# Optimization experiments

Hardware: AMD Instinct MI355X
Metric: run time of the kernel (lower is better)

## Reference

```python
import jax, jax.numpy as jnp
import numpy as np

N_NODES = 50000
N_EDGES = 1_600_000
IN_DIM = 128
HID = 32
HEADS = 4
NEG_SLOPE = 0.2


def setup_inputs() -> dict:
    key = jax.random.key(0)
    ks = jax.random.split(key, 6)
    h = jax.random.normal(ks[0], (N_NODES, IN_DIM), dtype=jnp.float32)
    src = jax.random.randint(ks[1], (N_EDGES,), 0, N_NODES, dtype=jnp.int32)
    dst = jax.random.randint(ks[2], (N_EDGES,), 0, N_NODES, dtype=jnp.int32)
    s = 1.0 / np.sqrt(IN_DIM)  # ~ Linear default init scale
    Wq = (jax.random.normal(ks[3], (HEADS, IN_DIM, HID), dtype=jnp.float32) * s)
    Wk = (jax.random.normal(ks[4], (HEADS, IN_DIM, HID), dtype=jnp.float32) * s)
    Wv = (jax.random.normal(ks[5], (HEADS, IN_DIM, HID), dtype=jnp.float32) * s)
    return {"h": h, "src": src, "dst": dst, "Wq": Wq, "Wk": Wk, "Wv": Wv}


def _gat_forward(h, src, dst, Wq, Wk, Wv):
    n = h.shape[0]
    # per-head projections: [H, N, D]
    q = jnp.einsum('ni,hio->hno', h, Wq)
    k = jnp.einsum('ni,hio->hno', h, Wk)
    v = jnp.einsum('ni,hio->hno', h, Wv)
    # edge scores: e = leaky_relu(<q_src, k_dst>)  -> [H, E]
    e = jax.nn.leaky_relu(jnp.einsum('hed,hed->he', q[:, src], k[:, dst]),
                          negative_slope=NEG_SLOPE)
    # segment softmax over incoming edges of each dst node
    seg_max = jax.vmap(lambda x: jax.ops.segment_max(x, dst, num_segments=n))(e)
    seg_max = jax.lax.stop_gradient(jnp.where(jnp.isfinite(seg_max), seg_max, 0.0))
    ex = jnp.exp(e - seg_max[:, dst])                       # [H, E]
    denom = jax.vmap(lambda x: jax.ops.segment_sum(x, dst, num_segments=n))(ex)
    alpha = ex / jnp.maximum(denom, 1e-9)[:, dst]           # [H, E]
    # weighted scatter-sum of source values into dst nodes: [H, N, D]
    msg = alpha[..., None] * v[:, src]
    out = jax.vmap(lambda m: jax.ops.segment_sum(m, dst, num_segments=n))(msg)
    # concat heads along feature dim -> [N, H*D]
    return out.transpose(1, 0, 2).reshape(n, HEADS * HID)


def reference(h, src, dst, Wq, Wk, Wv):
    return _gat_forward(h, src, dst, Wq, Wk, Wv)
```

## Files before the change

### kernel.cpp

```cpp
#include <hip/hip_runtime.h>
#include <hip/hip_fp16.h>

#define IN_DIM 128
#define HID 32
#define HEADS 4
#define OUTC (HEADS*HID)
#define NEG_SLOPE 0.2f
#define BSHIFT 7
#define BNODES 128
#define BCAP 6144
#define MAXBUCK 512
#define NCOLS 384
#define SUBN 16
#define SCAP 1024

typedef _Float16 f16x8 __attribute__((ext_vector_type(8)));
typedef float    f32x4 __attribute__((ext_vector_type(4)));

__device__ __forceinline__ unsigned short f2h(float f) {
    return __half_as_ushort(__float2half_rn(f));
}
__device__ __forceinline__ float2 h2f2(unsigned u) {
    __half2 h = *reinterpret_cast<__half2*>(&u);
    return __half22float2(h);
}
__device__ __forceinline__ float qdot(const uint4& qv, const float4& kd) {
    float2 a = h2f2(qv.x);
    float2 b = h2f2(qv.y);
    return a.x * kd.x + a.y * kd.y + b.x * kd.z + b.y * kd.w;
}
__device__ __forceinline__ void vacc(const uint4& qv, float e, float4& acc) {
    float2 a = h2f2(qv.z);
    float2 b = h2f2(qv.w);
    acc.x = fmaf(e, a.x, acc.x);
    acc.y = fmaf(e, a.y, acc.y);
    acc.z = fmaf(e, b.x, acc.z);
    acc.w = fmaf(e, b.y, acc.w);
}

__global__ __launch_bounds__(256) void w_prep(
    const float* __restrict__ Wq, const float* __restrict__ Wk,
    const float* __restrict__ Wv, unsigned short* __restrict__ Wt,
    int* __restrict__ gcount)
{
    int idx = blockIdx.x * 256 + threadIdx.x;
    if (idx < MAXBUCK) gcount[idx] = 0;
    if (idx >= NCOLS * IN_DIM) return;
    int c = idx >> 7, k = idx & 127;
    int sel = c >> 7;
    int cc  = c & 127;
    int head = cc >> 5, dcol = cc & 31;
    const float* W = (sel == 0) ? Wk : (sel == 1) ? Wq : Wv;
    Wt[idx] = f2h(W[(size_t)head * IN_DIM * HID + (size_t)k * HID + dcol]);
}

__global__ __launch_bounds__(256) void gat_proj_mfma(
    const float* __restrict__ h, const unsigned short* __restrict__ Wt,
    float* __restrict__ Ko, unsigned short* __restrict__ QV, int n)
{
    __shared__ unsigned short hsm[32 * IN_DIM];
    const int tid  = threadIdx.x;
    const int row0 = blockIdx.x * 32;

    for (int idx = tid; idx < 32 * 64; idx += 256) {
        int r  = idx >> 6;
        int c2 = idx & 63;
        int gr = row0 + r;
        float2 hv = (gr < n) ? ((const float2*)h)[(size_t)gr * 64 + c2]
                             : make_float2(0.f, 0.f);
        int col = c2 * 2;
        int sc  = col ^ ((r & 7) << 3);
        __half2 packed = __floats2half2_rn(hv.x, hv.y);
        *(unsigned*)&hsm[r * IN_DIM + sc] = *(unsigned*)&packed;
    }
    __syncthreads();

    const int w = tid >> 6;
    const int l = tid & 63;
    const int l15 = l & 15;
    const int kg  = l >> 4;
    const _Float16* Wt16 = (const _Float16*)Wt;

    f32x4 acc[2][6];
#pragma unroll
    for (int rt = 0; rt < 2; ++rt)
#pragma unroll
        for (int ct = 0; ct < 6; ++ct) acc[rt][ct] = (f32x4){0.f, 0.f, 0.f, 0.f};

#pragma unroll
    for (int s = 0; s < 4; ++s) {
        int scol = (s * 32 + kg * 8) ^ ((l & 7) << 3);
        f16x8 a0 = *(const f16x8*)&hsm[l15 * IN_DIM + scol];
        f16x8 a1 = *(const f16x8*)&hsm[(l15 + 16) * IN_DIM + scol];
#pragma unroll
        for (int ct = 0; ct < 6; ++ct) {
            int c = w * 96 + ct * 16 + l15;
            f16x8 b = *(const f16x8*)&Wt16[(size_t)c * IN_DIM + s * 32 + kg * 8];
            acc[0][ct] = __builtin_amdgcn_mfma_f32_16x16x32_f16(a0, b, acc[0][ct], 0, 0, 0);
            acc[1][ct] = __builtin_amdgcn_mfma_f32_16x16x32_f16(a1, b, acc[1][ct], 0, 0, 0);
        }
    }

#pragma unroll
    for (int rt = 0; rt < 2; ++rt) {
#pragma unroll
        for (int ct = 0; ct < 6; ++ct) {
            int cD = w * 96 + ct * 16 + l15;
#pragma unroll
            for (int r = 0; r < 4; ++r) {
                int node = row0 + rt * 16 + kg * 4 + r;
                if (node >= n) continue;
                float v = acc[rt][ct][r];
                if (cD < 128) {
                    Ko[(size_t)node * OUTC + cD] = v;
                } else if (cD < 256) {
                    int cq = cD - 128;
                    QV[(size_t)node * 256 + (cq >> 2) * 8 + (cq & 3)] = f2h(v);
                } else {
                    int cv = cD - 256;
                    QV[(size_t)node * 256 + (cv >> 2) * 8 + (cv & 3) + 4] = f2h(v);
                }
            }
        }
    }
}

__global__ __launch_bounds__(256) void gat_bin(
    const int* __restrict__ src, const int* __restrict__ dst,
    int* __restrict__ gcount, unsigned* __restrict__ pairs,
    int ne, int nbuck)
{
    __shared__ int hist[MAXBUCK];
    __shared__ int base[MAXBUCK];
    const int tid = threadIdx.x;
    for (int i = tid; i < nbuck; i += 256) hist[i] = 0;
    __syncthreads();

    const int ne4 = ne >> 2;
    const int4* s4 = (const int4*)src;
    const int4* d4 = (const int4*)dst;

    int4 sv[4], dv[4];
    int loc[16], bk[16];
    bool val[4];
#pragma unroll
    for (int k = 0; k < 4; ++k) {
        int idx = blockIdx.x * 1024 + k * 256 + tid;
        val[k] = idx < ne4;
        if (val[k]) { sv[k] = s4[idx]; dv[k] = d4[idx]; }
        else { sv[k] = make_int4(0,0,0,0); dv[k] = make_int4(0,0,0,0); }
    }
#pragma unroll
    for (int k = 0; k < 4; ++k) {
        int dd[4] = { dv[k].x, dv[k].y, dv[k].z, dv[k].w };
#pragma unroll
        for (int j = 0; j < 4; ++j) {
            int b = dd[j] >> BSHIFT;
            bk[k*4+j]  = b;
            loc[k*4+j] = val[k] ? atomicAdd(&hist[b], 1) : 0;
        }
    }
    __syncthreads();
    for (int i = tid; i < nbuck; i += 256)
        base[i] = hist[i] ? atomicAdd(&gcount[i], hist[i]) : 0;
    __syncthreads();
#pragma unroll
    for (int k = 0; k < 4; ++k) {
        if (!val[k]) continue;
        int ss[4] = { sv[k].x, sv[k].y, sv[k].z, sv[k].w };
        int dd[4] = { dv[k].x, dv[k].y, dv[k].z, dv[k].w };
#pragma unroll
        for (int j = 0; j < 4; ++j) {
            int b = bk[k*4+j];
            int p = base[b] + loc[k*4+j];
            if (p < BCAP)
                pairs[(size_t)b * BCAP + p] =
                    ((unsigned)ss[j] << BSHIFT) | (unsigned)(dd[j] & (BNODES-1));
        }
    }
    if (blockIdx.x == 0 && tid == 0) {
        for (int e = ne4 * 4; e < ne; ++e) {
            int b = dst[e] >> BSHIFT;
            int p = atomicAdd(&gcount[b], 1);
            if (p < BCAP)
                pairs[(size_t)b * BCAP + p] =
                    ((unsigned)src[e] << BSHIFT) | (unsigned)(dst[e] & (BNODES-1));
        }
    }
}

__global__ __launch_bounds__(256) void gat_bucket(
    const unsigned* __restrict__ pairs, const int* __restrict__ gcount,
    const uint4* __restrict__ QV, const float4* __restrict__ K4,
    float* __restrict__ out, int n, int nbuck)
{
    __shared__ unsigned short sl[SCAP];
    __shared__ int cl[SUBN], cur[SUBN], off[SUBN + 1];

    const int blk = blockIdx.x;
    const int sub = (blk >> 3) & 7;
    const int b   = (blk >> 6) * 8 + (blk & 7);
    if (b >= nbuck) return;
    const int tid = threadIdx.x;

    if (tid < SUBN) cl[tid] = 0;
    __syncthreads();

    int m = gcount[b]; if (m > BCAP) m = BCAP;
    const unsigned* pb = pairs + (size_t)b * BCAP;

    for (int i = tid; i < m; i += 256) {
        int dl = pb[i] & (BNODES - 1);
        if ((dl >> 4) == sub) atomicAdd(&cl[dl & (SUBN - 1)], 1);
    }
    __syncthreads();
    if (tid == 0) {
        int acc = 0;
#pragma unroll
        for (int i = 0; i < SUBN; ++i) { off[i] = acc; cur[i] = acc; acc += cl[i]; }
        off[SUBN] = acc;
    }
    __syncthreads();
    for (int i = tid; i < m; i += 256) {
        unsigned p = pb[i];
        int dl = p & (BNODES - 1);
        if ((dl >> 4) == sub) {
            int pos = atomicAdd(&cur[dl & (SUBN - 1)], 1);
            if (pos < SCAP) sl[pos] = (unsigned short)(p >> BSHIFT);
        }
    }
    __syncthreads();

    const int w    = tid >> 6;
    const int lane = tid & 63;
    const int l32  = lane & 31;
    const int g    = lane >> 5;

#pragma unroll
    for (int q = 0; q < SUBN / 4; ++q) {
        int nl   = q * 4 + w;
        int node = b * BNODES + sub * SUBN + nl;
        if (node >= n) continue;

        const int e0  = off[nl];
        const int deg = off[nl + 1] - e0;
        const float4 kd = K4[(size_t)node * 32 + l32];

        float4 acc = make_float4(0.f, 0.f, 0.f, 0.f);
        float  dsum = 0.f;

        const int half0 = (deg + 1) >> 1;
        int j  = e0 + (g ? half0 : 0);
        const int je = e0 + (g ? deg : half0);

        for (; j + 3 < je; j += 4) {
            int s0 = sl[j], s1 = sl[j + 1], s2 = sl[j + 2], s3 = sl[j + 3];
            uint4 w0 = QV[(size_t)s0 * 32 + l32];
            uint4 w1 = QV[(size_t)s1 * 32 + l32];
            uint4 w2 = QV[(size_t)s2 * 32 + l32];
            uint4 w3 = QV[(size_t)s3 * 32 + l32];

            float p0 = qdot(w0, kd), p1 = qdot(w1, kd);
            float p2 = qdot(w2, kd), p3 = qdot(w3, kd);
#pragma unroll
            for (int off2 = 1; off2 < 8; off2 <<= 1) {
                p0 += __shfl_xor(p0, off2, 8);
                p1 += __shfl_xor(p1, off2, 8);
                p2 += __shfl_xor(p2, off2, 8);
                p3 += __shfl_xor(p3, off2, 8);
            }
            float e0f = __expf(p0 > 0.f ? p0 : NEG_SLOPE * p0);
            float e1f = __expf(p1 > 0.f ? p1 : NEG_SLOPE * p1);
            float e2f = __expf(p2 > 0.f ? p2 : NEG_SLOPE * p2);
            float e3f = __expf(p3 > 0.f ? p3 : NEG_SLOPE * p3);
            dsum += (e0f + e1f) + (e2f + e3f);
            vacc(w0, e0f, acc); vacc(w1, e1f, acc);
            vacc(w2, e2f, acc); vacc(w3, e3f, acc);
        }
        for (; j < je; ++j) {
            int s0 = sl[j];
            uint4 w0 = QV[(size_t)s0 * 32 + l32];
            float p0 = qdot(w0, kd);
#pragma unroll
            for (int off2 = 1; off2 < 8; off2 <<= 1) p0 += __shfl_xor(p0, off2, 8);
            float e0f = __expf(p0 > 0.f ? p0 : NEG_SLOPE * p0);
            dsum += e0f;
            vacc(w0, e0f, acc);
        }

        acc.x += __shfl_xor(acc.x, 32, 64);
        acc.y += __shfl_xor(acc.y, 32, 64);
        acc.z += __shfl_xor(acc.z, 32, 64);
        acc.w += __shfl_xor(acc.w, 32, 64);
        dsum  += __shfl_xor(dsum, 32, 64);

        if (g == 0) {
            float inv = 1.f / fmaxf(dsum, 1e-9f);
            float4 o; o.x = acc.x*inv; o.y = acc.y*inv; o.z = acc.z*inv; o.w = acc.w*inv;
            ((float4*)out)[(size_t)node * 32 + l32] = o;
        }
    }
}

extern "C" void kernel_launch(void* const* d_in, const int* in_sizes, int n_in,
                              void* d_out, int out_size, void* d_ws, size_t ws_size,
                              hipStream_t stream) {
    const float* h   = (const float*)d_in[0];
    const int*   src = (const int*)d_in[1];
    const int*   dst = (const int*)d_in[2];
    const float* Wq  = (const float*)d_in[3];
    const float* Wk  = (const float*)d_in[4];
    const float* Wv  = (const float*)d_in[5];
    float* out = (float*)d_out;

    const int n     = in_sizes[0] / IN_DIM;
    const int ne    = in_sizes[1];
    const int nbuck = (n + BNODES - 1) >> BSHIFT;

    float*          K      = (float*)d_ws;
    unsigned short* QV     = (unsigned short*)(K + (size_t)n * OUTC);
    int*            gcount = (int*)(QV + (size_t)n * 256);
    unsigned*       pairs  = (unsigned*)(gcount + MAXBUCK);
    unsigned short* Wt     = (unsigned short*)(pairs + (size_t)MAXBUCK * BCAP);

    w_prep<<<(NCOLS * IN_DIM + 255) / 256, 256, 0, stream>>>(Wq, Wk, Wv, Wt, gcount);
    gat_proj_mfma<<<(n + 31) / 32, 256, 0, stream>>>(h, Wt, K, QV, n);

    int ne4 = ne >> 2;
    int binblk = (ne4 + 1023) / 1024;
    gat_bin<<<binblk, 256, 0, stream>>>(src, dst, gcount, pairs, ne, nbuck);

    int nb8  = (nbuck + 7) / 8;
    gat_bucket<<<nb8 * 64, 256, 0, stream>>>(pairs, gcount, (const uint4*)QV,
                                             (const float4*)K, out, n, nbuck);
}
```

Measured before the change: 183.7 us.

## Bin edges into 16-node buckets and fuse weight prep with binning

Edges are now binned directly into 16-node buckets (3125 buckets), so each gat_bucket block handles exactly one bucket. Before, each block rescanned a 128-node bucket and filtered for its 16-node sub-range, which made every bucket's pairs be read eight times. The weight conversion and the edge binning are merged into one launch, and the count reset moves to a memset. The cost is a larger shared histogram (3200 entries of hist plus base) and more global atomics on gcount during binning, which may lower occupancy in the binning blocks. The per-bucket capacity of 768 for 16 nodes averaging 512 edges leaves less slack for overflow.

```diff
diff --git a/kernel.cpp b/kernel.cpp
--- a/kernel.cpp
+++ b/kernel.cpp
@@ -6,13 +6,12 @@
 #define HEADS 4
 #define OUTC (HEADS*HID)
 #define NEG_SLOPE 0.2f
-#define BSHIFT 7
-#define BNODES 128
-#define BCAP 6144
-#define MAXBUCK 512
+#define BSH 4
+#define BN 16
+#define BCAP 768
+#define NBMAX 3200
 #define NCOLS 384
-#define SUBN 16
-#define SCAP 1024
+#define WPB 192
 
 typedef _Float16 f16x8 __attribute__((ext_vector_type(8)));
 typedef float    f32x4 __attribute__((ext_vector_type(4)));
@@ -38,20 +37,86 @@
     acc.w = fmaf(e, b.y, acc.w);
 }
 
-__global__ __launch_bounds__(256) void w_prep(
+__global__ __launch_bounds__(256) void prep_bin(
     const float* __restrict__ Wq, const float* __restrict__ Wk,
     const float* __restrict__ Wv, unsigned short* __restrict__ Wt,
-    int* __restrict__ gcount)
+    const int* __restrict__ src, const int* __restrict__ dst,
+    int* __restrict__ gcount, unsigned* __restrict__ pairs,
+    int ne, int nbuck)
 {
-    int idx = blockIdx.x * 256 + threadIdx.x;
-    if (idx < MAXBUCK) gcount[idx] = 0;
-    if (idx >= NCOLS * IN_DIM) return;
-    int c = idx >> 7, k = idx & 127;
-    int sel = c >> 7;
-    int cc  = c & 127;
-    int head = cc >> 5, dcol = cc & 31;
-    const float* W = (sel == 0) ? Wk : (sel == 1) ? Wq : Wv;
-    Wt[idx] = f2h(W[(size_t)head * IN_DIM * HID + (size_t)k * HID + dcol]);
+    const int tid = threadIdx.x;
+
+    if (blockIdx.x < WPB) {
+        int idx = blockIdx.x * 256 + tid;
+        if (idx < NCOLS * IN_DIM) {
+            int c = idx >> 7, k = idx & 127;
+            int sel = c >> 7;
+            int cc  = c & 127;
+            int head = cc >> 5, dcol = cc & 31;
+            const float* W = (sel == 0) ? Wk : (sel == 1) ? Wq : Wv;
+            Wt[idx] = f2h(W[(size_t)head * IN_DIM * HID + (size_t)k * HID + dcol]);
+        }
+        return;
+    }
+
+    __shared__ int hist[NBMAX];
+    __shared__ int base[NBMAX];
+    const int bblk = blockIdx.x - WPB;
+
+    for (int i = tid; i < nbuck; i += 256) hist[i] = 0;
+    __syncthreads();
+
+    const int ne4 = ne >> 2;
+    const int4* s4 = (const int4*)src;
+    const int4* d4 = (const int4*)dst;
+
+    int4 sv[4], dv[4];
+    int loc[16], bk[16];
+    bool val[4];
+#pragma unroll
+    for (int k = 0; k < 4; ++k) {
+        int idx = bblk * 1024 + k * 256 + tid;
+        val[k] = idx < ne4;
+        if (val[k]) { sv[k] = s4[idx]; dv[k] = d4[idx]; }
+        else { sv[k] = make_int4(0,0,0,0); dv[k] = make_int4(0,0,0,0); }
+    }
+#pragma unroll
+    for (int k = 0; k < 4; ++k) {
+        int dd[4] = { dv[k].x, dv[k].y, dv[k].z, dv[k].w };
+#pragma unroll
+        for (int j = 0; j < 4; ++j) {
+            int b = dd[j] >> BSH;
+            bk[k*4+j]  = b;
+            loc[k*4+j] = val[k] ? atomicAdd(&hist[b], 1) : 0;
+        }
+    }
+    __syncthreads();
+    for (int i = tid; i < nbuck; i += 256)
+        base[i] = hist[i] ? atomicAdd(&gcount[i], hist[i]) : 0;
+    __syncthreads();
+#pragma unroll
+    for (int k = 0; k < 4; ++k) {
+        if (!val[k]) continue;
+        int ss[4] = { sv[k].x, sv[k].y, sv[k].z, sv[k].w };
+        int dd[4] = { dv[k].x, dv[k].y, dv[k].z, dv[k].w };
+#pragma unroll
+        for (int j = 0; j < 4; ++j) {
+            int b = bk[k*4+j];
+            int p = base[b] + loc[k*4+j];
+            if (p < BCAP)
+                pairs[(size_t)b * BCAP + p] =
+                    ((unsigned)ss[j] << BSH) | (unsigned)(dd[j] & (BN-1));
+        }
+    }
+    if (bblk == 0 && tid == 0) {
+        for (int e = ne4 * 4; e < ne; ++e) {
+            int b = dst[e] >> BSH;
+            int p = atomicAdd(&gcount[b], 1);
+            if (p < BCAP)
+                pairs[(size_t)b * BCAP + p] =
+                    ((unsigned)src[e] << BSH) | (unsigned)(dst[e] & (BN-1));
+        }
+    }
 }
 
 __global__ __launch_bounds__(256) void gat_proj_mfma(
@@ -125,109 +190,37 @@
     }
 }
 
-__global__ __launch_bounds__(256) void gat_bin(
-    const int* __restrict__ src, const int* __restrict__ dst,
-    int* __restrict__ gcount, unsigned* __restrict__ pairs,
-    int ne, int nbuck)
-{
-    __shared__ int hist[MAXBUCK];
-    __shared__ int base[MAXBUCK];
-    const int tid = threadIdx.x;
-    for (int i = tid; i < nbuck; i += 256) hist[i] = 0;
-    __syncthreads();
-
-    const int ne4 = ne >> 2;
-    const int4* s4 = (const int4*)src;
-    const int4* d4 = (const int4*)dst;
-
-    int4 sv[4], dv[4];
-    int loc[16], bk[16];
-    bool val[4];
-#pragma unroll
-    for (int k = 0; k < 4; ++k) {
-        int idx = blockIdx.x * 1024 + k * 256 + tid;
-        val[k] = idx < ne4;
-        if (val[k]) { sv[k] = s4[idx]; dv[k] = d4[idx]; }
-        else { sv[k] = make_int4(0,0,0,0); dv[k] = make_int4(0,0,0,0); }
-    }
-#pragma unroll
-    for (int k = 0; k < 4; ++k) {
-        int dd[4] = { dv[k].x, dv[k].y, dv[k].z, dv[k].w };
-#pragma unroll
-        for (int j = 0; j < 4; ++j) {
-            int b = dd[j] >> BSHIFT;
-            bk[k*4+j]  = b;
-            loc[k*4+j] = val[k] ? atomicAdd(&hist[b], 1) : 0;
-        }
-    }
-    __syncthreads();
-    for (int i = tid; i < nbuck; i += 256)
-        base[i] = hist[i] ? atomicAdd(&gcount[i], hist[i]) : 0;
-    __syncthreads();
-#pragma unroll
-    for (int k = 0; k < 4; ++k) {
-        if (!val[k]) continue;
-        int ss[4] = { sv[k].x, sv[k].y, sv[k].z, sv[k].w };
-        int dd[4] = { dv[k].x, dv[k].y, dv[k].z, dv[k].w };
-#pragma unroll
-        for (int j = 0; j < 4; ++j) {
-            int b = bk[k*4+j];
-            int p = base[b] + loc[k*4+j];
-            if (p < BCAP)
-                pairs[(size_t)b * BCAP + p] =
-                    ((unsigned)ss[j] << BSHIFT) | (unsigned)(dd[j] & (BNODES-1));
-        }
-    }
-    if (blockIdx.x == 0 && tid == 0) {
-        for (int e = ne4 * 4; e < ne; ++e) {
-            int b = dst[e] >> BSHIFT;
-            int p = atomicAdd(&gcount[b], 1);
-            if (p < BCAP)
-                pairs[(size_t)b * BCAP + p] =
-                    ((unsigned)src[e] << BSHIFT) | (unsigned)(dst[e] & (BNODES-1));
-        }
-    }
-}
-
 __global__ __launch_bounds__(256) void gat_bucket(
     const unsigned* __restrict__ pairs, const int* __restrict__ gcount,
     const uint4* __restrict__ QV, const float4* __restrict__ K4,
     float* __restrict__ out, int n, int nbuck)
 {
-    __shared__ unsigned short sl[SCAP];
-    __shared__ int cl[SUBN], cur[SUBN], off[SUBN + 1];
-
-    const int blk = blockIdx.x;
-    const int sub = (blk >> 3) & 7;
-    const int b   = (blk >> 6) * 8 + (blk & 7);
+    __shared__ unsigned short sl[BCAP];
+    __shared__ int cl[BN], cur[BN], off[BN + 1];
+
+    const int b   = blockIdx.x;
     if (b >= nbuck) return;
     const int tid = threadIdx.x;
 
-    if (tid < SUBN) cl[tid] = 0;
+    if (tid < BN) cl[tid] = 0;
     __syncthreads();
 
     int m = gcount[b]; if (m > BCAP) m = BCAP;
     const unsigned* pb = pairs + (size_t)b * BCAP;
 
-    for (int i = tid; i < m; i += 256) {
-        int dl = pb[i] & (BNODES - 1);
-        if ((dl >> 4) == sub) atomicAdd(&cl[dl & (SUBN - 1)], 1);
-    }
+    for (int i = tid; i < m; i += 256) atomicAdd(&cl[pb[i] & (BN - 1)], 1);
     __syncthreads();
     if (tid == 0) {
         int acc = 0;
 #pragma unroll
-        for (int i = 0; i < SUBN; ++i) { off[i] = acc; cur[i] = acc; acc += cl[i]; }
-        off[SUBN] = acc;
+        for (int i = 0; i < BN; ++i) { off[i] = acc; cur[i] = acc; acc += cl[i]; }
+        off[BN] = acc;
     }
     __syncthreads();
     for (int i = tid; i < m; i += 256) {
         unsigned p = pb[i];
-        int dl = p & (BNODES - 1);
-        if ((dl >> 4) == sub) {
-            int pos = atomicAdd(&cur[dl & (SUBN - 1)], 1);
-            if (pos < SCAP) sl[pos] = (unsigned short)(p >> BSHIFT);
-        }
+        int pos = atomicAdd(&cur[p & (BN - 1)], 1);
+        sl[pos] = (unsigned short)(p >> BSH);
     }
     __syncthreads();
 
@@ -237,9 +230,9 @@
     const int g    = lane >> 5;
 
 #pragma unroll
-    for (int q = 0; q < SUBN / 4; ++q) {
+    for (int q = 0; q < BN / 4; ++q) {
         int nl   = q * 4 + w;
-        int node = b * BNODES + sub * SUBN + nl;
+        int node = b * BN + nl;
         if (node >= n) continue;
 
         const int e0  = off[nl];
@@ -315,22 +308,23 @@
 
     const int n     = in_sizes[0] / IN_DIM;
     const int ne    = in_sizes[1];
-    const int nbuck = (n + BNODES - 1) >> BSHIFT;
+    const int nbuck = (n + BN - 1) >> BSH;
 
     float*          K      = (float*)d_ws;
     unsigned short* QV     = (unsigned short*)(K + (size_t)n * OUTC);
     int*            gcount = (int*)(QV + (size_t)n * 256);
-    unsigned*       pairs  = (unsigned*)(gcount + MAXBUCK);
-    unsigned short* Wt     = (unsigned short*)(pairs + (size_t)MAXBUCK * BCAP);
-
-    w_prep<<<(NCOLS * IN_DIM + 255) / 256, 256, 0, stream>>>(Wq, Wk, Wv, Wt, gcount);
-    gat_proj_mfma<<<(n + 31) / 32, 256, 0, stream>>>(h, Wt, K, QV, n);
+    unsigned*       pairs  = (unsigned*)(gcount + NBMAX);
+    unsigned short* Wt     = (unsigned short*)(pairs + (size_t)NBMAX * BCAP);
+
+    hipMemsetAsync(gcount, 0, NBMAX * sizeof(int), stream);
 
     int ne4 = ne >> 2;
     int binblk = (ne4 + 1023) / 1024;
-    gat_bin<<<binblk, 256, 0, stream>>>(src, dst, gcount, pairs, ne, nbuck);
-
-    int nb8  = (nbuck + 7) / 8;
-    gat_bucket<<<nb8 * 64, 256, 0, stream>>>(pairs, gcount, (const uint4*)QV,
-                                             (const float4*)K, out, n, nbuck);
-}
+    prep_bin<<<WPB + binblk, 256, 0, stream>>>(Wq, Wk, Wv, Wt, src, dst,
+                                               gcount, pairs, ne, nbuck);
+
+    gat_proj_mfma<<<(n + 31) / 32, 256, 0, stream>>>(h, Wt, K, QV, n);
+
+    gat_bucket<<<nbuck, 256, 0, stream>>>(pairs, gcount, (const uint4*)QV,
+                                          (const float4*)K, out, n, nbuck);
+}
```

Result: no change. 186.9 us (+1.8%).
